# Performance work log

Hardware: AMD Instinct MI355X
Metric: run time of the kernel (lower is better)

## Reference

```python
import jax, jax.numpy as jnp
import numpy as np


def _conv1d_block(x, W, b):
    # reflection pad 1 each side, conv1d k=3 stride=2, relu
    x = jnp.pad(x, ((0, 0), (0, 0), (1, 1)), mode='reflect')
    y = jax.lax.conv_general_dilated(x, W, window_strides=(2,), padding='VALID',
                                     dimension_numbers=('NCH', 'OIH', 'NCH'))
    return jax.nn.relu(y + b[None, :, None])


def setup_inputs() -> dict:
    key = jax.random.key(0)
    ks = jax.random.split(key, 8)
    C, H, E, P = 62, 256, 1024, 32768
    inp = {
        'image_x': jax.random.normal(ks[0], (C, H, H), dtype=jnp.float32),
        'corners': jax.random.uniform(ks[1], (E, 2), dtype=jnp.float32),
        'W0': jax.random.normal(ks[2], (64, C + 2, 3), dtype=jnp.float32) * 0.02,
        'b0': jnp.zeros((64,), jnp.float32),
        'W1': jax.random.normal(ks[3], (64, 64, 3), dtype=jnp.float32) * 0.02,
        'b1': jnp.zeros((64,), jnp.float32),
        'W2': jax.random.normal(ks[4], (64, 64, 3), dtype=jnp.float32) * 0.02,
        'b2': jnp.zeros((64,), jnp.float32),
        'Wf': jax.random.normal(ks[5], (64, 64), dtype=jnp.float32) * 0.05,
        'bf': jnp.zeros((64,), jnp.float32),
        'Wp': jax.random.normal(ks[6], (1, 64), dtype=jnp.float32) * 0.05,
        'bp': jnp.zeros((1,), jnp.float32),
        'num_points': P,  # static stand-in for the host-synced data-dependent count
    }
    return inp


def reference(image_x, corners, W0, b0, W1, b1, W2, b2, Wf, bf, Wp, bp, num_points):
    # edges: [E,4] = (start_xy, end_xy) with wraparound
    edges = jnp.concatenate([corners, jnp.roll(corners, -1, axis=0)], axis=-1)
    starts, ends = edges[:, :2], edges[:, 2:4]
    dirs = ends - starts                                  # [E,2]
    lengths = jnp.linalg.norm(dirs, axis=-1)              # [E]
    length_sum = lengths.sum()
    # arc-length sample offsets (num_points is static)
    offsets = jnp.arange(num_points, dtype=jnp.float32) * (length_sum / num_points)  # [P]
    el2 = jnp.cumsum(lengths)                             # [E]
    el1 = jnp.concatenate([jnp.zeros((1,), lengths.dtype), el2[:-1]])
    # per-(point, edge) interpolation parameter and bin mask
    t = (offsets[:, None] - el1[None, :]) / jnp.maximum(lengths, 1e-4)[None, :]      # [P,E]
    mask = ((offsets[:, None] >= el1[None, :]) & (offsets[:, None] < el2[None, :])).astype(jnp.float32)
    # masked reduction: sum_e mask*(start + t*dir)  (same math, no [P,E,2] temp)
    points = jnp.einsum('pe,ec->pc', mask, starts) + jnp.einsum('pe,ec->pc', mask * t, dirs)  # [P,2]
    H = image_x.shape[1]
    pr = jnp.clip(jnp.round(points * H).astype(jnp.int32), 0, H - 1)  # [P,2]
    x = image_x[:, pr[:, 0], pr[:, 1]]                    # [C,P] fancy gather
    x = jnp.concatenate([x, points.T], axis=0)[None]      # [1,C+2,P]
    x = _conv1d_block(x, W0, b0)
    x = _conv1d_block(x, W1, b1)
    x = _conv1d_block(x, W2, b2)
    x = x.max(axis=-1)                                    # [1,64]
    feat = jax.nn.relu(x @ Wf.T + bf)                     # [1,64]
    pred = jax.nn.sigmoid(feat @ Wp.T + bp).reshape(-1)   # [1]
    return feat, pred
```

## Files before the change

### kernel.cpp

```cpp
#include <hip/hip_runtime.h>
#include <hip/hip_bf16.h>
#include <math.h>

#define EDGES   32768
#define NPTS    32768
#define IMGH    256
#define L0      32768
#define L1      16384
#define L2      8192
#define L3      4096
#define S0      (L1 + 64)
#define NBC     133

#define P4_SCAN 128
#define P4_W    18
#define P4_T    1024
#define P4_GRID (P4_SCAN + P4_W + P4_T)

__device__ __forceinline__ void stage_ws(float ws[96][64],
                                         const float* __restrict__ Wsrc, int tid)
{
    const float4* src = (const float4*)Wsrc;
    float4 rw[6];
#pragma unroll
    for (int k = 0; k < 6; ++k) rw[k] = src[k * 256 + tid];
    float4* dst = (float4*)&ws[0][0];
#pragma unroll
    for (int k = 0; k < 6; ++k) dst[k * 256 + tid] = rw[k];
}

__device__ __forceinline__ void conv_half(float acc[16],
                                          const float xs[64][130],
                                          const float ws[96][64],
                                          int ibase, int jl2, int o0)
{
#pragma unroll 4
    for (int ii = 0; ii < 32; ++ii) {
        int i = ibase + ii;
        float x0 = xs[i][jl2], x1 = xs[i][jl2 + 1], x2 = xs[i][jl2 + 2];
        const float4* w0 = (const float4*)&ws[ii*3 + 0][o0];
        const float4* w1 = (const float4*)&ws[ii*3 + 1][o0];
        const float4* w2 = (const float4*)&ws[ii*3 + 2][o0];
#pragma unroll
        for (int q = 0; q < 4; ++q) {
            float4 a = w0[q], b = w1[q], c = w2[q];
            acc[q*4+0] = fmaf(a.x, x0, fmaf(b.x, x1, fmaf(c.x, x2, acc[q*4+0])));
            acc[q*4+1] = fmaf(a.y, x0, fmaf(b.y, x1, fmaf(c.y, x2, acc[q*4+1])));
            acc[q*4+2] = fmaf(a.z, x0, fmaf(b.z, x1, fmaf(c.z, x2, acc[q*4+2])));
            acc[q*4+3] = fmaf(a.w, x0, fmaf(b.w, x1, fmaf(c.w, x2, acc[q*4+3])));
        }
    }
}

__global__ __launch_bounds__(256) void prep4_k(const float* __restrict__ corners,
                                               const float* __restrict__ W0,
                                               const float* __restrict__ W1,
                                               const float* __restrict__ W2,
                                               const float* __restrict__ img,
                                               double* __restrict__ el2loc,
                                               double* __restrict__ partial,
                                               float*  __restrict__ Wt,
                                               float*  __restrict__ imgT)
{
    __shared__ union {
        double sc[256];
        float  tt[64][68];
    } sm;
    int b = blockIdx.x, t = threadIdx.x;

    if (b < P4_SCAN) {
        int e  = (b << 8) + t;
        int en = (e + 1) & (EDGES - 1);
        double dx = (double)corners[2*en]   - (double)corners[2*e];
        double dy = (double)corners[2*en+1] - (double)corners[2*e+1];
        sm.sc[t] = sqrt(dx*dx + dy*dy);
        __syncthreads();
        for (int o = 1; o < 256; o <<= 1) {
            double v = (t >= o) ? sm.sc[t - o] : 0.0;
            __syncthreads();
            sm.sc[t] += v;
            __syncthreads();
        }
        el2loc[e] = sm.sc[t];
        if (t == 255) partial[b] = sm.sc[255];
    } else if (b < P4_SCAN + P4_W) {
        int wb = b - P4_SCAN;
#pragma unroll
        for (int k = 0; k < 8; ++k) {
            int idx = wb*2048 + k*256 + t;
            int l   = idx / 12288;
            int rem = idx - l * 12288;
            int row = rem >> 6, o = rem & 63;
            int i   = row / 3,  kk = row - i * 3;
            const float* W = (l == 0) ? W0 : ((l == 1) ? W1 : W2);
            Wt[idx] = W[o*192 + i*3 + kk];
        }
    } else {
        int tb   = b - (P4_SCAN + P4_W);
        int pix0 = tb << 6;
        const float4* img4 = (const float4*)img;
#pragma unroll
        for (int k = 0; k < 4; ++k) {
            int idx = k*256 + t;
            if (idx < 992) {
                int c = idx >> 4, p4 = idx & 15;
                float4 v = img4[c*16384 + (pix0 >> 2) + p4];
                sm.tt[p4*4 + 0][c] = v.x;
                sm.tt[p4*4 + 1][c] = v.y;
                sm.tt[p4*4 + 2][c] = v.z;
                sm.tt[p4*4 + 3][c] = v.w;
            }
        }
        __syncthreads();
        float4* imgT4 = (float4*)imgT;
#pragma unroll
        for (int k = 0; k < 4; ++k) {
            int idx = k*256 + t;
            int p = idx >> 4, c4 = idx & 15;
            if (c4 < 15) {
                float4 v = *(const float4*)&sm.tt[p][c4*4];
                imgT4[((size_t)(pix0 + p) << 4) + c4] = v;
            } else {
                float2 v = make_float2(sm.tt[p][60], sm.tt[p][61]);
                *(float2*)(imgT + ((size_t)(pix0 + p) << 6) + 60) = v;
            }
        }
    }
}

__global__ __launch_bounds__(256) void convA4_k(const float* __restrict__ corners,
                                                const double* __restrict__ el2loc,
                                                const double* __restrict__ partial,
                                                const float* __restrict__ imgT,
                                                const float* __restrict__ Wt,
                                                const float* __restrict__ b0v,
                                                float* __restrict__ Y0)
{
    __shared__ float  xs[64][130];
    __shared__ float  ws[96][64];
    __shared__ double sb[128];
    int tid = threadIdx.x;
    int b   = blockIdx.x;
    int j0  = b << 6;
    int in0 = (j0 << 1) - 1;

    if (tid < 128) sb[tid] = partial[tid];
    __syncthreads();
#pragma unroll
    for (int o = 1; o < 128; o <<= 1) {
        double v = 0.0;
        if (tid < 128 && tid >= o) v = sb[tid - o];
        __syncthreads();
        if (tid < 128) sb[tid] += v;
        __syncthreads();
    }

    stage_ws(ws, Wt, tid);

    if (tid < 130) {
        int g = in0 + tid;
        if (g < 0)   g = 1;
        if (g >= L0) g = 2*L0 - 2 - g;
        double S   = sb[127];
        double off = (double)g * (S * (1.0 / (double)NPTS));
        int clo = 0, chi = 127;
        while (clo < chi) { int cm = (clo + chi) >> 1;
                            if (sb[cm] > off) chi = cm; else clo = cm + 1; }
        double base = clo ? sb[clo - 1] : 0.0;
        int lo = clo << 8, hi = lo + 255;
        while (lo < hi) { int mid = (lo + hi) >> 1;
                          if (el2loc[mid] + base > off) hi = mid; else lo = mid + 1; }
        int e = lo;
        double e1 = (e == 0) ? 0.0
                  : el2loc[e-1] + (((e-1) >= 256) ? sb[((e-1) >> 8) - 1] : 0.0);
        float sxf = corners[2*e], syf = corners[2*e+1];
        int en = (e + 1) & (EDGES - 1);
        double dx = (double)corners[2*en]   - (double)sxf;
        double dy = (double)corners[2*en+1] - (double)syf;
        double len = sqrt(dx*dx + dy*dy);
        double tp  = (off - e1) / fmax(len, 0.0001);
        double px  = (double)sxf + tp * dx;
        double py  = (double)syf + tp * dy;
        int r0 = (int)rint(px * (double)IMGH); r0 = r0 < 0 ? 0 : (r0 > IMGH-1 ? IMGH-1 : r0);
        int r1 = (int)rint(py * (double)IMGH); r1 = r1 < 0 ? 0 : (r1 > IMGH-1 ? IMGH-1 : r1);
        const float4* row4 = (const float4*)(imgT + ((size_t)((r0 << 8) | r1) << 6));
        float4 rv[15];
#pragma unroll
        for (int c4 = 0; c4 < 15; ++c4) rv[c4] = row4[c4];
        float c60 = ((const float*)row4)[60], c61 = ((const float*)row4)[61];
#pragma unroll
        for (int c4 = 0; c4 < 15; ++c4) {
            xs[c4*4 + 0][tid] = rv[c4].x;
            xs[c4*4 + 1][tid] = rv[c4].y;
            xs[c4*4 + 2][tid] = rv[c4].z;
            xs[c4*4 + 3][tid] = rv[c4].w;
        }
        xs[60][tid] = c60;
        xs[61][tid] = c61;
        xs[62][tid] = (float)px;
        xs[63][tid] = (float)py;
    }
    __syncthreads();

    int lane = tid & 63;
    int o0   = (tid >> 6) << 4;
    float acc[16];
#pragma unroll
    for (int m = 0; m < 16; ++m) acc[m] = b0v[o0 + m];
    int jl2 = lane << 1;

    conv_half(acc, xs, ws, 0, jl2, o0);
    __syncthreads();
    stage_ws(ws, Wt + 96*64, tid);
    __syncthreads();
    conv_half(acc, xs, ws, 32, jl2, o0);

    int j = j0 + lane;
#pragma unroll
    for (int m = 0; m < 16; ++m)
        Y0[(o0 + m) * S0 + j] = fmaxf(acc[m], 0.f);
}

__global__ __launch_bounds__(256) void convBC_k(const float* __restrict__ Y0,
                                                const float* __restrict__ Wt1,
                                                const float* __restrict__ b1,
                                                const float* __restrict__ Wt2,
                                                const float* __restrict__ b2,
                                                float* __restrict__ pmax)
{
    __shared__ float xs0[32][132];
    __shared__ float t1[64][63];
    __shared__ float ws[96][64];
    int tid = threadIdx.x;
    int b   = blockIdx.x;
    int gbase = 124*b - 3;

    int s  = tid & 63;
    int o0 = (tid >> 6) << 4;
    int j1 = 62*b - 1 + s;
    int jr = (j1 < 0) ? -j1 : (j1 > L2-1 ? L2-1 : j1);
    int col0 = 2*jr - 124*b + 2;

    {
        float r[16];
#pragma unroll
        for (int k = 0; k < 16; ++k) {
            int idx = k*256 + tid;
            int c   = idx >> 7, col = idx & 127;
            int g   = gbase + col;
            if (g < 0)   g = -g;
            if (g >= L1) g = 2*L1 - 2 - g;
            r[k] = Y0[c * S0 + g];
        }
        stage_ws(ws, Wt1, tid);
#pragma unroll
        for (int k = 0; k < 16; ++k) {
            int idx = k*256 + tid;
            xs0[idx >> 7][idx & 127] = r[k];
        }
    }
    __syncthreads();

    float acc1[16];
#pragma unroll
    for (int m = 0; m < 16; ++m) acc1[m] = b1[o0 + m];
#pragma unroll 4
    for (int ii = 0; ii < 32; ++ii) {
        float x0 = xs0[ii][col0], x1 = xs0[ii][col0+1], x2 = xs0[ii][col0+2];
        const float4* w0 = (const float4*)&ws[ii*3 + 0][o0];
        const float4* w1 = (const float4*)&ws[ii*3 + 1][o0];
        const float4* w2 = (const float4*)&ws[ii*3 + 2][o0];
#pragma unroll
        for (int q = 0; q < 4; ++q) {
            float4 a = w0[q], bb = w1[q], c = w2[q];
            acc1[q*4+0] = fmaf(a.x, x0, fmaf(bb.x, x1, fmaf(c.x, x2, acc1[q*4+0])));
            acc1[q*4+1] = fmaf(a.y, x0, fmaf(bb.y, x1, fmaf(c.y, x2, acc1[q*4+1])));
            acc1[q*4+2] = fmaf(a.z, x0, fmaf(bb.z, x1, fmaf(c.z, x2, acc1[q*4+2])));
            acc1[q*4+3] = fmaf(a.w, x0, fmaf(bb.w, x1, fmaf(c.w, x2, acc1[q*4+3])));
        }
    }
    __syncthreads();
    {
        float r[16];
#pragma unroll
        for (int k = 0; k < 16; ++k) {
            int idx = k*256 + tid;
            int c   = idx >> 7, col = idx & 127;
            int g   = gbase + col;
            if (g < 0)   g = -g;
            if (g >= L1) g = 2*L1 - 2 - g;
            r[k] = Y0[(32 + c) * S0 + g];
        }
        stage_ws(ws, Wt1 + 96*64, tid);
#pragma unroll
        for (int k = 0; k < 16; ++k) {
            int idx = k*256 + tid;
            xs0[idx >> 7][idx & 127] = r[k];
        }
    }
    __syncthreads();
#pragma unroll 4
    for (int ii = 0; ii < 32; ++ii) {
        float x0 = xs0[ii][col0], x1 = xs0[ii][col0+1], x2 = xs0[ii][col0+2];
        const float4* w0 = (const float4*)&ws[ii*3 + 0][o0];
        const float4* w1 = (const float4*)&ws[ii*3 + 1][o0];
        const float4* w2 = (const float4*)&ws[ii*3 + 2][o0];
#pragma unroll
        for (int q = 0; q < 4; ++q) {
            float4 a = w0[q], bb = w1[q], c = w2[q];
            acc1[q*4+0] = fmaf(a.x, x0, fmaf(bb.x, x1, fmaf(c.x, x2, acc1[q*4+0])));
            acc1[q*4+1] = fmaf(a.y, x0, fmaf(bb.y, x1, fmaf(c.y, x2, acc1[q*4+1])));
            acc1[q*4+2] = fmaf(a.z, x0, fmaf(bb.z, x1, fmaf(c.z, x2, acc1[q*4+2])));
            acc1[q*4+3] = fmaf(a.w, x0, fmaf(bb.w, x1, fmaf(c.w, x2, acc1[q*4+3])));
        }
    }
    __syncthreads();
    if (s < 63) {
#pragma unroll
        for (int m = 0; m < 16; ++m) t1[o0 + m][s] = fmaxf(acc1[m], 0.f);
    }
    __syncthreads();

    int p  = tid & 31;
    int oc = (tid >> 5) << 3;
    float acc2[8];
#pragma unroll
    for (int q = 0; q < 8; ++q) acc2[q] = b2[oc + q];

    stage_ws(ws, Wt2, tid);
    __syncthreads();
#pragma unroll 4
    for (int ii = 0; ii < 32; ++ii) {
        float x0 = t1[ii][2*p + 0], x1 = t1[ii][2*p + 1], x2 = t1[ii][2*p + 2];
        const float4* w0 = (const float4*)&ws[ii*3 + 0][oc];
        const float4* w1 = (const float4*)&ws[ii*3 + 1][oc];
        const float4* w2 = (const float4*)&ws[ii*3 + 2][oc];
#pragma unroll
        for (int q4 = 0; q4 < 2; ++q4) {
            float4 a = w0[q4], bb = w1[q4], c = w2[q4];
            acc2[q4*4+0] = fmaf(a.x, x0, fmaf(bb.x, x1, fmaf(c.x, x2, acc2[q4*4+0])));
            acc2[q4*4+1] = fmaf(a.y, x0, fmaf(bb.y, x1, fmaf(c.y, x2, acc2[q4*4+1])));
            acc2[q4*4+2] = fmaf(a.z, x0, fmaf(bb.z, x1, fmaf(c.z, x2, acc2[q4*4+2])));
            acc2[q4*4+3] = fmaf(a.w, x0, fmaf(bb.w, x1, fmaf(c.w, x2, acc2[q4*4+3])));
        }
    }
    __syncthreads();
    stage_ws(ws, Wt2 + 96*64, tid);
    __syncthreads();
#pragma unroll 4
    for (int ii = 0; ii < 32; ++ii) {
        float x0 = t1[32+ii][2*p + 0], x1 = t1[32+ii][2*p + 1], x2 = t1[32+ii][2*p + 2];
        const float4* w0 = (const float4*)&ws[ii*3 + 0][oc];
        const float4* w1 = (const float4*)&ws[ii*3 + 1][oc];
        const float4* w2 = (const float4*)&ws[ii*3 + 2][oc];
#pragma unroll
        for (int q4 = 0; q4 < 2; ++q4) {
            float4 a = w0[q4], bb = w1[q4], c = w2[q4];
            acc2[q4*4+0] = fmaf(a.x, x0, fmaf(bb.x, x1, fmaf(c.x, x2, acc2[q4*4+0])));
            acc2[q4*4+1] = fmaf(a.y, x0, fmaf(bb.y, x1, fmaf(c.y, x2, acc2[q4*4+1])));
            acc2[q4*4+2] = fmaf(a.z, x0, fmaf(bb.z, x1, fmaf(c.z, x2, acc2[q4*4+2])));
            acc2[q4*4+3] = fmaf(a.w, x0, fmaf(bb.w, x1, fmaf(c.w, x2, acc2[q4*4+3])));
        }
    }

    bool valid = (p < 31) && (31*b + p < L3);
#pragma unroll
    for (int q = 0; q < 8; ++q) {
        float v = valid ? fmaxf(acc2[q], 0.f) : 0.f;
#pragma unroll
        for (int off = 1; off < 32; off <<= 1)
            v = fmaxf(v, __shfl_xor(v, off));
        if (p == 0) pmax[b * 64 + oc + q] = v;
    }
}

__global__ __launch_bounds__(256) void fc_k(const float* __restrict__ pmax,
                                            const float* __restrict__ Wf,
                                            const float* __restrict__ bf,
                                            const float* __restrict__ Wp,
                                            const float* __restrict__ bp,
                                            float* __restrict__ out)
{
    __shared__ float red[4][64];
    __shared__ float cm[64];
    __shared__ float ft[64];
    int t  = threadIdx.x;
    int ch = t & 63;
    int q  = t >> 6;
    float m = 0.f;
    for (int b = q; b < NBC; b += 4) m = fmaxf(m, pmax[b * 64 + ch]);
    red[q][ch] = m;
    __syncthreads();
    if (t < 64) {
        cm[t] = fmaxf(fmaxf(red[0][t], red[1][t]), fmaxf(red[2][t], red[3][t]));
    }
    __syncthreads();
    if (t < 64) {
        float s = bf[t];
#pragma unroll
        for (int c = 0; c < 64; ++c) s = fmaf(Wf[t*64 + c], cm[c], s);
        float f = fmaxf(s, 0.f);
        ft[t] = f;
        out[t] = f;
    }
    __syncthreads();
    if (t == 0) {
        float z = bp[0];
#pragma unroll
        for (int c = 0; c < 64; ++c) z = fmaf(Wp[c], ft[c], z);
        out[64] = 1.f / (1.f + expf(-z));
    }
}

extern "C" void kernel_launch(void* const* d_in, const int* in_sizes, int n_in,
                              void* d_out, int out_size, void* d_ws, size_t ws_size,
                              hipStream_t stream)
{
    const float* image   = (const float*)d_in[0];
    const float* corners = (const float*)d_in[1];
    const float* W0      = (const float*)d_in[2];
    const float* b0      = (const float*)d_in[3];
    const float* W1      = (const float*)d_in[4];
    const float* b1      = (const float*)d_in[5];
    const float* W2      = (const float*)d_in[6];
    const float* b2      = (const float*)d_in[7];
    const float* Wf      = (const float*)d_in[8];
    const float* bf      = (const float*)d_in[9];
    const float* Wp      = (const float*)d_in[10];
    const float* bp      = (const float*)d_in[11];
    float* out = (float*)d_out;

    char* w = (char*)d_ws;
    double* el2loc  = (double*)(w);
    double* partial = (double*)(w + 262144);
    float*  pmax    = (float*) (w + 263168);
    float*  Wt      = (float*) (w + 297216);
    float*  imgT    = (float*) (w + 444672);
    float*  Y0      = (float*) (w + 17221888);

    prep4_k  <<<P4_GRID, 256, 0, stream>>>(corners, W0, W1, W2, image,
                                           el2loc, partial, Wt, imgT);
    convA4_k <<<256, 256, 0, stream>>>(corners, el2loc, partial, imgT, Wt, b0, Y0);
    convBC_k <<<NBC, 256, 0, stream>>>(Y0, Wt + 12288, b1, Wt + 24576, b2, pmax);
    fc_k     <<<1, 256, 0, stream>>>(pmax, Wf, bf, Wp, bp, out);
}
```

Baseline: 57.89 us.

## Split conv B/C across 256 blocks and fuse FC head via last-block ticket

Conv layers 1 and 2 are retiled so each block produces 32 layer-2 outputs instead of 62. The grid grows from 133 to 256 blocks so more compute units are busy. The separate FC kernel is removed: each block bumps an atomic counter (reset in prep4_k), and the last block to finish reduces pmax and computes the FC and sigmoid outputs. This saves a kernel launch and raises parallelism, at the cost of more halo redundancy and a serialized tail in the last block.

```diff
diff --git a/kernel.cpp b/kernel.cpp
--- a/kernel.cpp
+++ b/kernel.cpp
@@ -10,7 +10,6 @@
 #define L2      8192
 #define L3      4096
 #define S0      (L1 + 64)
-#define NBC     133
 
 #define P4_SCAN 128
 #define P4_W    18
@@ -60,7 +59,8 @@
                                                double* __restrict__ el2loc,
                                                double* __restrict__ partial,
                                                float*  __restrict__ Wt,
-                                               float*  __restrict__ imgT)
+                                               float*  __restrict__ imgT,
+                                               unsigned* __restrict__ done)
 {
     __shared__ union {
         double sc[256];
@@ -85,6 +85,7 @@
         if (t == 255) partial[b] = sm.sc[255];
     } else if (b < P4_SCAN + P4_W) {
         int wb = b - P4_SCAN;
+        if (wb == 0 && t == 0) *done = 0u;
 #pragma unroll
         for (int k = 0; k < 8; ++k) {
             int idx = wb*2048 + k*256 + t;
@@ -221,32 +222,42 @@
         Y0[(o0 + m) * S0 + j] = fmaxf(acc[m], 0.f);
 }
 
-__global__ __launch_bounds__(256) void convBC_k(const float* __restrict__ Y0,
-                                                const float* __restrict__ Wt1,
-                                                const float* __restrict__ b1,
-                                                const float* __restrict__ Wt2,
-                                                const float* __restrict__ b2,
-                                                float* __restrict__ pmax)
-{
-    __shared__ float xs0[32][132];
-    __shared__ float t1[64][63];
+__global__ __launch_bounds__(256) void convBC256_k(const float* __restrict__ Y0,
+                                                   const float* __restrict__ Wt1,
+                                                   const float* __restrict__ b1,
+                                                   const float* __restrict__ Wt2,
+                                                   const float* __restrict__ b2,
+                                                   const float* __restrict__ Wf,
+                                                   const float* __restrict__ bf,
+                                                   const float* __restrict__ Wp,
+                                                   const float* __restrict__ bp,
+                                                   float* __restrict__ pmax,
+                                                   unsigned* __restrict__ done,
+                                                   float* __restrict__ out)
+{
+    __shared__ float xs0[32][76];
+    __shared__ float t1[64][34];
     __shared__ float ws[96][64];
+    __shared__ float red[4][64];
+    __shared__ float cm[64], ft[64];
+    __shared__ unsigned ticket;
     int tid = threadIdx.x;
     int b   = blockIdx.x;
-    int gbase = 124*b - 3;
+    int gbase = 64*b - 4;
 
     int s  = tid & 63;
     int o0 = (tid >> 6) << 4;
-    int j1 = 62*b - 1 + s;
+    int j1 = 32*b - 1 + s;
     int jr = (j1 < 0) ? -j1 : (j1 > L2-1 ? L2-1 : j1);
-    int col0 = 2*jr - 124*b + 2;
+    int col0 = 2*jr - 64*b + 3;
+    col0 = col0 > 69 ? 69 : col0;
 
     {
-        float r[16];
-#pragma unroll
-        for (int k = 0; k < 16; ++k) {
+        float r[9];
+#pragma unroll
+        for (int k = 0; k < 9; ++k) {
             int idx = k*256 + tid;
-            int c   = idx >> 7, col = idx & 127;
+            int c   = idx / 72, col = idx - 72*c;
             int g   = gbase + col;
             if (g < 0)   g = -g;
             if (g >= L1) g = 2*L1 - 2 - g;
@@ -254,9 +265,10 @@
         }
         stage_ws(ws, Wt1, tid);
 #pragma unroll
-        for (int k = 0; k < 16; ++k) {
+        for (int k = 0; k < 9; ++k) {
             int idx = k*256 + tid;
-            xs0[idx >> 7][idx & 127] = r[k];
+            int c   = idx / 72, col = idx - 72*c;
+            xs0[c][col] = r[k];
         }
     }
     __syncthreads();
@@ -272,20 +284,20 @@
         const float4* w2 = (const float4*)&ws[ii*3 + 2][o0];
 #pragma unroll
         for (int q = 0; q < 4; ++q) {
-            float4 a = w0[q], bb = w1[q], c = w2[q];
-            acc1[q*4+0] = fmaf(a.x, x0, fmaf(bb.x, x1, fmaf(c.x, x2, acc1[q*4+0])));
-            acc1[q*4+1] = fmaf(a.y, x0, fmaf(bb.y, x1, fmaf(c.y, x2, acc1[q*4+1])));
-            acc1[q*4+2] = fmaf(a.z, x0, fmaf(bb.z, x1, fmaf(c.z, x2, acc1[q*4+2])));
-            acc1[q*4+3] = fmaf(a.w, x0, fmaf(bb.w, x1, fmaf(c.w, x2, acc1[q*4+3])));
+            float4 a = w0[q], bw = w1[q], c = w2[q];
+            acc1[q*4+0] = fmaf(a.x, x0, fmaf(bw.x, x1, fmaf(c.x, x2, acc1[q*4+0])));
+            acc1[q*4+1] = fmaf(a.y, x0, fmaf(bw.y, x1, fmaf(c.y, x2, acc1[q*4+1])));
+            acc1[q*4+2] = fmaf(a.z, x0, fmaf(bw.z, x1, fmaf(c.z, x2, acc1[q*4+2])));
+            acc1[q*4+3] = fmaf(a.w, x0, fmaf(bw.w, x1, fmaf(c.w, x2, acc1[q*4+3])));
         }
     }
     __syncthreads();
     {
-        float r[16];
-#pragma unroll
-        for (int k = 0; k < 16; ++k) {
+        float r[9];
+#pragma unroll
+        for (int k = 0; k < 9; ++k) {
             int idx = k*256 + tid;
-            int c   = idx >> 7, col = idx & 127;
+            int c   = idx / 72, col = idx - 72*c;
             int g   = gbase + col;
             if (g < 0)   g = -g;
             if (g >= L1) g = 2*L1 - 2 - g;
@@ -293,9 +305,10 @@
         }
         stage_ws(ws, Wt1 + 96*64, tid);
 #pragma unroll
-        for (int k = 0; k < 16; ++k) {
+        for (int k = 0; k < 9; ++k) {
             int idx = k*256 + tid;
-            xs0[idx >> 7][idx & 127] = r[k];
+            int c   = idx / 72, col = idx - 72*c;
+            xs0[c][col] = r[k];
         }
     }
     __syncthreads();
@@ -307,42 +320,38 @@
         const float4* w2 = (const float4*)&ws[ii*3 + 2][o0];
 #pragma unroll
         for (int q = 0; q < 4; ++q) {
-            float4 a = w0[q], bb = w1[q], c = w2[q];
-            acc1[q*4+0] = fmaf(a.x, x0, fmaf(bb.x, x1, fmaf(c.x, x2, acc1[q*4+0])));
-            acc1[q*4+1] = fmaf(a.y, x0, fmaf(bb.y, x1, fmaf(c.y, x2, acc1[q*4+1])));
-            acc1[q*4+2] = fmaf(a.z, x0, fmaf(bb.z, x1, fmaf(c.z, x2, acc1[q*4+2])));
-            acc1[q*4+3] = fmaf(a.w, x0, fmaf(bb.w, x1, fmaf(c.w, x2, acc1[q*4+3])));
-        }
-    }
-    __syncthreads();
-    if (s < 63) {
+            float4 a = w0[q], bw = w1[q], c = w2[q];
+            acc1[q*4+0] = fmaf(a.x, x0, fmaf(bw.x, x1, fmaf(c.x, x2, acc1[q*4+0])));
+            acc1[q*4+1] = fmaf(a.y, x0, fmaf(bw.y, x1, fmaf(c.y, x2, acc1[q*4+1])));
+            acc1[q*4+2] = fmaf(a.z, x0, fmaf(bw.z, x1, fmaf(c.z, x2, acc1[q*4+2])));
+            acc1[q*4+3] = fmaf(a.w, x0, fmaf(bw.w, x1, fmaf(c.w, x2, acc1[q*4+3])));
+        }
+    }
+    __syncthreads();
+    if (s < 33) {
 #pragma unroll
         for (int m = 0; m < 16; ++m) t1[o0 + m][s] = fmaxf(acc1[m], 0.f);
     }
     __syncthreads();
 
-    int p  = tid & 31;
-    int oc = (tid >> 5) << 3;
-    float acc2[8];
-#pragma unroll
-    for (int q = 0; q < 8; ++q) acc2[q] = b2[oc + q];
+    int p  = tid & 15;
+    int oc = (tid >> 4) << 2;
+    float acc2[4];
+#pragma unroll
+    for (int q = 0; q < 4; ++q) acc2[q] = b2[oc + q];
 
     stage_ws(ws, Wt2, tid);
     __syncthreads();
 #pragma unroll 4
     for (int ii = 0; ii < 32; ++ii) {
         float x0 = t1[ii][2*p + 0], x1 = t1[ii][2*p + 1], x2 = t1[ii][2*p + 2];
-        const float4* w0 = (const float4*)&ws[ii*3 + 0][oc];
-        const float4* w1 = (const float4*)&ws[ii*3 + 1][oc];
-        const float4* w2 = (const float4*)&ws[ii*3 + 2][oc];
-#pragma unroll
-        for (int q4 = 0; q4 < 2; ++q4) {
-            float4 a = w0[q4], bb = w1[q4], c = w2[q4];
-            acc2[q4*4+0] = fmaf(a.x, x0, fmaf(bb.x, x1, fmaf(c.x, x2, acc2[q4*4+0])));
-            acc2[q4*4+1] = fmaf(a.y, x0, fmaf(bb.y, x1, fmaf(c.y, x2, acc2[q4*4+1])));
-            acc2[q4*4+2] = fmaf(a.z, x0, fmaf(bb.z, x1, fmaf(c.z, x2, acc2[q4*4+2])));
-            acc2[q4*4+3] = fmaf(a.w, x0, fmaf(bb.w, x1, fmaf(c.w, x2, acc2[q4*4+3])));
-        }
+        float4 a  = *(const float4*)&ws[ii*3 + 0][oc];
+        float4 bw = *(const float4*)&ws[ii*3 + 1][oc];
+        float4 c  = *(const float4*)&ws[ii*3 + 2][oc];
+        acc2[0] = fmaf(a.x, x0, fmaf(bw.x, x1, fmaf(c.x, x2, acc2[0])));
+        acc2[1] = fmaf(a.y, x0, fmaf(bw.y, x1, fmaf(c.y, x2, acc2[1])));
+        acc2[2] = fmaf(a.z, x0, fmaf(bw.z, x1, fmaf(c.z, x2, acc2[2])));
+        acc2[3] = fmaf(a.w, x0, fmaf(bw.w, x1, fmaf(c.w, x2, acc2[3])));
     }
     __syncthreads();
     stage_ws(ws, Wt2 + 96*64, tid);
@@ -350,65 +359,55 @@
 #pragma unroll 4
     for (int ii = 0; ii < 32; ++ii) {
         float x0 = t1[32+ii][2*p + 0], x1 = t1[32+ii][2*p + 1], x2 = t1[32+ii][2*p + 2];
-        const float4* w0 = (const float4*)&ws[ii*3 + 0][oc];
-        const float4* w1 = (const float4*)&ws[ii*3 + 1][oc];
-        const float4* w2 = (const float4*)&ws[ii*3 + 2][oc];
-#pragma unroll
-        for (int q4 = 0; q4 < 2; ++q4) {
-            float4 a = w0[q4], bb = w1[q4], c = w2[q4];
-            acc2[q4*4+0] = fmaf(a.x, x0, fmaf(bb.x, x1, fmaf(c.x, x2, acc2[q4*4+0])));
-            acc2[q4*4+1] = fmaf(a.y, x0, fmaf(bb.y, x1, fmaf(c.y, x2, acc2[q4*4+1])));
-            acc2[q4*4+2] = fmaf(a.z, x0, fmaf(bb.z, x1, fmaf(c.z, x2, acc2[q4*4+2])));
-            acc2[q4*4+3] = fmaf(a.w, x0, fmaf(bb.w, x1, fmaf(c.w, x2, acc2[q4*4+3])));
-        }
-    }
-
-    bool valid = (p < 31) && (31*b + p < L3);
-#pragma unroll
-    for (int q = 0; q < 8; ++q) {
-        float v = valid ? fmaxf(acc2[q], 0.f) : 0.f;
-#pragma unroll
-        for (int off = 1; off < 32; off <<= 1)
+        float4 a  = *(const float4*)&ws[ii*3 + 0][oc];
+        float4 bw = *(const float4*)&ws[ii*3 + 1][oc];
+        float4 c  = *(const float4*)&ws[ii*3 + 2][oc];
+        acc2[0] = fmaf(a.x, x0, fmaf(bw.x, x1, fmaf(c.x, x2, acc2[0])));
+        acc2[1] = fmaf(a.y, x0, fmaf(bw.y, x1, fmaf(c.y, x2, acc2[1])));
+        acc2[2] = fmaf(a.z, x0, fmaf(bw.z, x1, fmaf(c.z, x2, acc2[2])));
+        acc2[3] = fmaf(a.w, x0, fmaf(bw.w, x1, fmaf(c.w, x2, acc2[3])));
+    }
+
+#pragma unroll
+    for (int q = 0; q < 4; ++q) {
+        float v = fmaxf(acc2[q], 0.f);
+#pragma unroll
+        for (int off = 1; off < 16; off <<= 1)
             v = fmaxf(v, __shfl_xor(v, off));
         if (p == 0) pmax[b * 64 + oc + q] = v;
     }
-}
-
-__global__ __launch_bounds__(256) void fc_k(const float* __restrict__ pmax,
-                                            const float* __restrict__ Wf,
-                                            const float* __restrict__ bf,
-                                            const float* __restrict__ Wp,
-                                            const float* __restrict__ bp,
-                                            float* __restrict__ out)
-{
-    __shared__ float red[4][64];
-    __shared__ float cm[64];
-    __shared__ float ft[64];
-    int t  = threadIdx.x;
-    int ch = t & 63;
-    int q  = t >> 6;
-    float m = 0.f;
-    for (int b = q; b < NBC; b += 4) m = fmaxf(m, pmax[b * 64 + ch]);
-    red[q][ch] = m;
-    __syncthreads();
-    if (t < 64) {
-        cm[t] = fmaxf(fmaxf(red[0][t], red[1][t]), fmaxf(red[2][t], red[3][t]));
-    }
-    __syncthreads();
-    if (t < 64) {
-        float s = bf[t];
-#pragma unroll
-        for (int c = 0; c < 64; ++c) s = fmaf(Wf[t*64 + c], cm[c], s);
-        float f = fmaxf(s, 0.f);
-        ft[t] = f;
-        out[t] = f;
-    }
-    __syncthreads();
-    if (t == 0) {
-        float z = bp[0];
-#pragma unroll
-        for (int c = 0; c < 64; ++c) z = fmaf(Wp[c], ft[c], z);
-        out[64] = 1.f / (1.f + expf(-z));
+
+    __threadfence();
+    __syncthreads();
+    if (tid == 0) ticket = atomicAdd(done, 1u);
+    __syncthreads();
+    if (ticket == 255) {
+        __threadfence();
+        int ch = tid & 63;
+        int qq = tid >> 6;
+        float m = 0.f;
+        for (int q = qq; q < 256; q += 4) m = fmaxf(m, pmax[q * 64 + ch]);
+        red[qq][ch] = m;
+        __syncthreads();
+        if (tid < 64)
+            cm[tid] = fmaxf(fmaxf(red[0][tid], red[1][tid]),
+                            fmaxf(red[2][tid], red[3][tid]));
+        __syncthreads();
+        if (tid < 64) {
+            float sfc = bf[tid];
+#pragma unroll
+            for (int c = 0; c < 64; ++c) sfc = fmaf(Wf[tid*64 + c], cm[c], sfc);
+            float f = fmaxf(sfc, 0.f);
+            ft[tid] = f;
+            out[tid] = f;
+        }
+        __syncthreads();
+        if (tid == 0) {
+            float z = bp[0];
+#pragma unroll
+            for (int c = 0; c < 64; ++c) z = fmaf(Wp[c], ft[c], z);
+            out[64] = 1.f / (1.f + expf(-z));
+        }
     }
 }
 
@@ -431,16 +430,17 @@
     float* out = (float*)d_out;
 
     char* w = (char*)d_ws;
-    double* el2loc  = (double*)(w);
-    double* partial = (double*)(w + 262144);
-    float*  pmax    = (float*) (w + 263168);
-    float*  Wt      = (float*) (w + 297216);
-    float*  imgT    = (float*) (w + 444672);
-    float*  Y0      = (float*) (w + 17221888);
-
-    prep4_k  <<<P4_GRID, 256, 0, stream>>>(corners, W0, W1, W2, image,
-                                           el2loc, partial, Wt, imgT);
-    convA4_k <<<256, 256, 0, stream>>>(corners, el2loc, partial, imgT, Wt, b0, Y0);
-    convBC_k <<<NBC, 256, 0, stream>>>(Y0, Wt + 12288, b1, Wt + 24576, b2, pmax);
-    fc_k     <<<1, 256, 0, stream>>>(pmax, Wf, bf, Wp, bp, out);
-}
+    double*   el2loc  = (double*)  (w);
+    double*   partial = (double*)  (w + 262144);
+    unsigned* done    = (unsigned*)(w + 263168);
+    float*    pmax    = (float*)   (w + 263424);
+    float*    Wt      = (float*)   (w + 328960);
+    float*    imgT    = (float*)   (w + 476416);
+    float*    Y0      = (float*)   (w + 17253632);
+
+    prep4_k    <<<P4_GRID, 256, 0, stream>>>(corners, W0, W1, W2, image,
+                                             el2loc, partial, Wt, imgT, done);
+    convA4_k   <<<256, 256, 0, stream>>>(corners, el2loc, partial, imgT, Wt, b0, Y0);
+    convBC256_k<<<256, 256, 0, stream>>>(Y0, Wt + 12288, b1, Wt + 24576, b2,
+                                         Wf, bf, Wp, bp, pmax, done, out);
+}
```

Measured after the change: 79.93 us. 1.38x slower.
